# Kernel tuning notes

Hardware: AMD Instinct MI355X
Metric: run time of the kernel (lower is better)

## Reference

```python
import jax, jax.numpy as jnp
import numpy as np

B, Dx, Dz, Dy, H = 4096, 512, 512, 256, 2048
T0, T1 = 0.0, 1.0
N_STEPS = 64


def setup_inputs() -> dict:
    key = jax.random.key(0)
    ks = jax.random.split(key, 9)
    X = jax.random.normal(ks[0], (B, Dx), jnp.float32)
    # P sampled Uniform(0.01, 0.1) as in the torch module
    P = jax.random.uniform(ks[1], (Dz, Dx), jnp.float32, 0.01, 0.1)
    # A scaled so spectral radius ~1 -> exp(A*T) stays bounded over the integration
    A = jax.random.normal(ks[2], (Dz, Dz), jnp.float32) * (Dz ** -0.5)
    W1 = jax.random.normal(ks[3], (H, Dz), jnp.float32) * (Dz ** -0.5)
    b1 = jax.random.normal(ks[4], (H,), jnp.float32) * 0.01
    W2 = jax.random.normal(ks[5], (H, H), jnp.float32) * (H ** -0.5)
    b2 = jax.random.normal(ks[6], (H,), jnp.float32) * 0.01
    W3 = jax.random.normal(ks[7], (Dy, H), jnp.float32) * (H ** -0.5)
    b3 = jax.random.normal(ks[8], (Dy,), jnp.float32) * 0.01
    return dict(X=X, P=P, A=A, W1=W1, b1=b1, W2=W2, b2=b2, W3=W3, b3=b3,
                n_steps=N_STEPS)


def reference(X, P, A, W1, b1, W2, b2, W3, b3, n_steps):
    # Z0 = einsum('ji,bi->bj', P, X)  -> projection into latent ODE state
    z0 = X @ P.T  # [B, Dz]
    dt = jnp.float32((T1 - T0) / n_steps)

    def f(z):  # dz/dt = A z, batched: einsum('ji,bi->bj', A, z)
        return z @ A.T

    def rk4_step(z, _):
        k1 = f(z)
        k2 = f(z + 0.5 * dt * k1)
        k3 = f(z + 0.5 * dt * k2)
        k4 = f(z + dt * k3)
        return z + (dt / 6.0) * (k1 + 2.0 * k2 + 2.0 * k3 + k4), None

    zT, _ = jax.lax.scan(rk4_step, z0, None, length=n_steps)  # [B, Dz]

    # QnnMatrixODE MLP head (n_layers=3): Lin+ReLU, Lin+ReLU, Lin
    h = jax.nn.relu(zT @ W1.T + b1)
    h = jax.nn.relu(h @ W2.T + b2)
    y = h @ W3.T + b3  # [B, Dy]
    return y
```

## Files before the change

### kernel.cpp

```cpp
#include <hip/hip_runtime.h>

#define BDIM 4096
#define DX 512
#define DZ 512
#define DY 256
#define HD 2048
#define LDT 72

typedef __attribute__((ext_vector_type(8))) short bf16x8;
typedef __attribute__((ext_vector_type(4))) float f32x4;

__device__ inline unsigned short f2bf(float f) {
    unsigned u = __float_as_uint(f);
    unsigned r = 0x7FFFu + ((u >> 16) & 1u);
    return (unsigned short)((u + r) >> 16);
}
__device__ inline float bf2f(unsigned short h) {
    return __uint_as_float(((unsigned)h) << 16);
}

#define GLDS16(g, l)                                                            \
    __builtin_amdgcn_global_load_lds((const __attribute__((address_space(1))) void*)(g), \
                                     (__attribute__((address_space(3))) void*)(l), 16, 0, 0)

struct PrepJobs {
    const float* src[7];
    unsigned short* hi[7];
    unsigned short* lo[7];
    int n4[7];
};
__global__ __launch_bounds__(256) void prep_k(PrepJobs J) {
    const int j = blockIdx.y;
    if (j < 6) {
        const int i4 = blockIdx.x * 256 + threadIdx.x;
        if (i4 >= J.n4[j]) return;
        float4 v = ((const float4*)J.src[j])[i4];
        ushort4 h;
        h.x = f2bf(v.x); h.y = f2bf(v.y); h.z = f2bf(v.z); h.w = f2bf(v.w);
        ((ushort4*)J.hi[j])[i4] = h;
        if (J.lo[j]) {
            ushort4 l;
            l.x = f2bf(v.x - bf2f(h.x));
            l.y = f2bf(v.y - bf2f(h.y));
            l.z = f2bf(v.z - bf2f(h.z));
            l.w = f2bf(v.w - bf2f(h.w));
            ((ushort4*)J.lo[j])[i4] = l;
        }
    } else {
        if (blockIdx.x >= 256) return;
        __shared__ float t[32][33];
        const float* A = J.src[6];
        unsigned short* HT = J.hi[6];
        unsigned short* LT = J.lo[6];
        const int bx = (blockIdx.x & 15) * 32, by = (blockIdx.x >> 4) * 32;
        const int x = threadIdx.x & 31, y = threadIdx.x >> 5;
#pragma unroll
        for (int dy = 0; dy < 32; dy += 8)
            t[y + dy][x] = A[(size_t)(by + y + dy) * DZ + bx + x];
        __syncthreads();
#pragma unroll
        for (int dy = 0; dy < 32; dy += 8) {
            float v = t[x][y + dy];
            unsigned short h = f2bf(v);
            size_t o = (size_t)(bx + y + dy) * DZ + by + x;
            HT[o] = h;
            LT[o] = f2bf(v - bf2f(h));
        }
    }
}

struct G64In { const unsigned short *Ahi, *Alo, *Bhi, *Blo; const float* Dadd; };
struct G64Out { float* Cf32; unsigned short *Chi, *Clo, *CThi, *CTlo; };
struct E0Out {
    const float* Af32;
    const unsigned short *A2h, *A2l;
    unsigned short *B0Th, *B0Tl, *B1Th, *B1Tl, *B2Th, *B2Tl;
};

template <int EPI>
__device__ __forceinline__ void g64_core(int bx, int by, int M, int N, int K,
                                         G64In in, G64Out o, E0Out e,
                                         unsigned short* Ash, unsigned short* Asl,
                                         unsigned short* Bsh, unsigned short* Bsl) {
    const int tid = threadIdx.x;
    const int lane = tid & 63;
    const int wave = tid >> 6;
    const int wr = wave >> 1, wc = wave & 1;
    const int row0 = by * 64, col0 = bx * 64;
    const int sr = tid >> 2;
    const int sk = (tid & 3) * 16;

    const int niter = K >> 6;
    bf16x8 pa0, pa1, pl0, pl1, pb0, pb1, pq0, pq1;
    {
        const unsigned short* ar = in.Ahi + (size_t)(row0 + sr) * K + sk;
        const unsigned short* al = in.Alo + (size_t)(row0 + sr) * K + sk;
        const unsigned short* br = in.Bhi + (size_t)(col0 + sr) * K + sk;
        const unsigned short* bl = in.Blo + (size_t)(col0 + sr) * K + sk;
        pa0 = *(const bf16x8*)ar; pa1 = *(const bf16x8*)(ar + 8);
        pl0 = *(const bf16x8*)al; pl1 = *(const bf16x8*)(al + 8);
        pb0 = *(const bf16x8*)br; pb1 = *(const bf16x8*)(br + 8);
        pq0 = *(const bf16x8*)bl; pq1 = *(const bf16x8*)(bl + 8);
    }

    f32x4 acc[4] = {};
    const int mb = wr * 32 + (lane & 15);
    const int nb = wc * 32 + (lane & 15);

    for (int it = 0; it < niter; ++it) {
        __syncthreads();
        *(bf16x8*)&Ash[sr * LDT + sk] = pa0; *(bf16x8*)&Ash[sr * LDT + sk + 8] = pa1;
        *(bf16x8*)&Asl[sr * LDT + sk] = pl0; *(bf16x8*)&Asl[sr * LDT + sk + 8] = pl1;
        *(bf16x8*)&Bsh[sr * LDT + sk] = pb0; *(bf16x8*)&Bsh[sr * LDT + sk + 8] = pb1;
        *(bf16x8*)&Bsl[sr * LDT + sk] = pq0; *(bf16x8*)&Bsl[sr * LDT + sk + 8] = pq1;
        __syncthreads();

        {
            const int kn = (it + 1 < niter) ? ((it + 1) << 6) : 0;
            const unsigned short* ar = in.Ahi + (size_t)(row0 + sr) * K + kn + sk;
            const unsigned short* al = in.Alo + (size_t)(row0 + sr) * K + kn + sk;
            const unsigned short* br = in.Bhi + (size_t)(col0 + sr) * K + kn + sk;
            const unsigned short* bl = in.Blo + (size_t)(col0 + sr) * K + kn + sk;
            pa0 = *(const bf16x8*)ar; pa1 = *(const bf16x8*)(ar + 8);
            pl0 = *(const bf16x8*)al; pl1 = *(const bf16x8*)(al + 8);
            pb0 = *(const bf16x8*)br; pb1 = *(const bf16x8*)(br + 8);
            pq0 = *(const bf16x8*)bl; pq1 = *(const bf16x8*)(bl + 8);
        }

#pragma unroll
        for (int kh = 0; kh < 2; ++kh) {
            const int kk = kh * 32 + (lane >> 4) * 8;
            bf16x8 ah[2], alx[2], bh[2], blx[2];
#pragma unroll
            for (int t = 0; t < 2; ++t) {
                ah[t]  = *(const bf16x8*)&Ash[(mb + t * 16) * LDT + kk];
                alx[t] = *(const bf16x8*)&Asl[(mb + t * 16) * LDT + kk];
                bh[t]  = *(const bf16x8*)&Bsh[(nb + t * 16) * LDT + kk];
                blx[t] = *(const bf16x8*)&Bsl[(nb + t * 16) * LDT + kk];
            }
#pragma unroll
            for (int mt = 0; mt < 2; ++mt)
#pragma unroll
                for (int nt = 0; nt < 2; ++nt) {
                    acc[mt * 2 + nt] = __builtin_amdgcn_mfma_f32_16x16x32_bf16(
                        ah[mt], bh[nt], acc[mt * 2 + nt], 0, 0, 0);
                    acc[mt * 2 + nt] = __builtin_amdgcn_mfma_f32_16x16x32_bf16(
                        ah[mt], blx[nt], acc[mt * 2 + nt], 0, 0, 0);
                    acc[mt * 2 + nt] = __builtin_amdgcn_mfma_f32_16x16x32_bf16(
                        alx[mt], bh[nt], acc[mt * 2 + nt], 0, 0, 0);
                }
        }
    }

#pragma unroll
    for (int mt = 0; mt < 2; ++mt) {
        const int grow = row0 + wr * 32 + mt * 16 + (lane >> 4) * 4;
#pragma unroll
        for (int nt = 0; nt < 2; ++nt) {
            const int gcol = col0 + wc * 32 + nt * 16 + (lane & 15);
            f32x4 a = acc[mt * 2 + nt];
            if (EPI == 1) {
                ushort4 h0, l0, h1v, l1v, h2v, l2v;
                unsigned short* H0 = &h0.x;  unsigned short* L0 = &l0.x;
                unsigned short* H1 = &h1v.x; unsigned short* L1 = &l1v.x;
                unsigned short* H2 = &h2v.x; unsigned short* L2 = &l2v.x;
#pragma unroll
                for (int i = 0; i < 4; ++i) {
                    const size_t idx = (size_t)(grow + i) * N + gcol;
                    const float di = (grow + i == gcol) ? 1.0f : 0.0f;
                    const float av = e.Af32[idx];
                    const float a2v = bf2f(e.A2h[idx]) + bf2f(e.A2l[idx]);
                    const float a3v = a[i];
                    float b0 = di + av + 0.5f * a2v + 1.6666667e-1f * a3v;
                    float b1 = 4.1666668e-2f * di + 8.3333333e-3f * av +
                               1.3888889e-3f * a2v + 1.9841270e-4f * a3v;
                    float b2 = 2.4801587e-5f * di + 2.7557319e-6f * av +
                               2.7557319e-7f * a2v + 2.5052108e-8f * a3v;
                    H0[i] = f2bf(b0); L0[i] = f2bf(b0 - bf2f(H0[i]));
                    H1[i] = f2bf(b1); L1[i] = f2bf(b1 - bf2f(H1[i]));
                    H2[i] = f2bf(b2); L2[i] = f2bf(b2 - bf2f(H2[i]));
                }
                const size_t to = (size_t)gcol * DZ + grow;
                *(ushort4*)&e.B0Th[to] = h0; *(ushort4*)&e.B0Tl[to] = l0;
                *(ushort4*)&e.B1Th[to] = h1v; *(ushort4*)&e.B1Tl[to] = l1v;
                *(ushort4*)&e.B2Th[to] = h2v; *(ushort4*)&e.B2Tl[to] = l2v;
            } else {
                if (in.Dadd) {
#pragma unroll
                    for (int i = 0; i < 4; ++i)
                        a[i] += in.Dadd[(size_t)(grow + i) * N + gcol];
                }
                unsigned short h4[4], l4[4];
#pragma unroll
                for (int i = 0; i < 4; ++i) {
                    h4[i] = f2bf(a[i]);
                    l4[i] = f2bf(a[i] - bf2f(h4[i]));
                }
                if (o.Cf32) {
#pragma unroll
                    for (int i = 0; i < 4; ++i) o.Cf32[(size_t)(grow + i) * N + gcol] = a[i];
                }
                if (o.Chi) {
#pragma unroll
                    for (int i = 0; i < 4; ++i) o.Chi[(size_t)(grow + i) * N + gcol] = h4[i];
                }
                if (o.Clo) {
#pragma unroll
                    for (int i = 0; i < 4; ++i) o.Clo[(size_t)(grow + i) * N + gcol] = l4[i];
                }
                if (o.CThi) {
                    ushort4 u = {h4[0], h4[1], h4[2], h4[3]};
                    *(ushort4*)&o.CThi[(size_t)gcol * M + grow] = u;
                }
                if (o.CTlo) {
                    ushort4 u = {l4[0], l4[1], l4[2], l4[3]};
                    *(ushort4*)&o.CTlo[(size_t)gcol * M + grow] = u;
                }
            }
        }
    }
}

__global__ __launch_bounds__(256) void g64_one(G64In in, G64Out o, int M, int N, int K) {
    __shared__ __align__(16) unsigned short Ash[64 * LDT], Asl[64 * LDT];
    __shared__ __align__(16) unsigned short Bsh[64 * LDT], Bsl[64 * LDT];
    E0Out e = {};
    g64_core<0>(blockIdx.x, blockIdx.y, M, N, K, in, o, e, Ash, Asl, Bsh, Bsl);
}

__global__ __launch_bounds__(256) void g64_dual_e0(G64In i0, E0Out e0o,
                                                   G64In i1, G64Out o1) {
    __shared__ __align__(16) unsigned short Ash[64 * LDT], Asl[64 * LDT];
    __shared__ __align__(16) unsigned short Bsh[64 * LDT], Bsl[64 * LDT];
    if (blockIdx.z == 0) {
        G64Out on = {};
        g64_core<1>(blockIdx.x, blockIdx.y, DZ, DZ, DZ, i0, on, e0o, Ash, Asl, Bsh, Bsl);
    } else {
        E0Out en = {};
        g64_core<0>(blockIdx.x, blockIdx.y, DZ, DZ, DZ, i1, o1, en, Ash, Asl, Bsh, Bsl);
    }
}

__global__ __launch_bounds__(256) void g64_tri(G64In i0, G64Out o0, G64In i1, G64Out o1,
                                               G64In i2, G64Out o2, int M, int N, int K) {
    __shared__ __align__(16) unsigned short Ash[64 * LDT], Asl[64 * LDT];
    __shared__ __align__(16) unsigned short Bsh[64 * LDT], Bsl[64 * LDT];
    E0Out e = {};
    G64In in = (blockIdx.z == 0) ? i0 : (blockIdx.z == 1) ? i1 : i2;
    G64Out o = (blockIdx.z == 0) ? o0 : (blockIdx.z == 1) ? o1 : o2;
    g64_core<0>(blockIdx.x, blockIdx.y, M, N, K, in, o, e, Ash, Asl, Bsh, Bsl);
}

template <int RELU, int BIAS, int OUT_BF16>
__global__ __launch_bounds__(256) void gemm_bf16_v2(int M, int N, int K,
                                                    const unsigned short* __restrict__ A,
                                                    const unsigned short* __restrict__ B,
                                                    void* __restrict__ C,
                                                    const float* __restrict__ bias) {
    __shared__ unsigned short As[64 * 32];
    __shared__ unsigned short Bs[128 * 32];

    const int tid = threadIdx.x;
    const int lane = tid & 63;
    const int wave = tid >> 6;
    const int wr = wave >> 1, wc = wave & 1;
    const int row0 = blockIdx.y * 64;
    const int col0 = blockIdx.x * 128;

    const int srow = lane >> 2;
    const int schunk = (lane & 3) * 8;

    f32x4 acc[2][4] = {};

    for (int k0 = 0; k0 < K; k0 += 32) {
        GLDS16(A + (size_t)(row0 + wave * 16 + srow) * K + k0 + schunk, &As[(wave * 16) * 32]);
        GLDS16(B + (size_t)(col0 + wave * 32 + srow) * K + k0 + schunk, &Bs[(wave * 32) * 32]);
        GLDS16(B + (size_t)(col0 + wave * 32 + 16 + srow) * K + k0 + schunk,
               &Bs[(wave * 32 + 16) * 32]);
        __syncthreads();

        const int kk = (lane >> 4) * 8;
        const int mbase = wr * 32 + (lane & 15);
        const int nbase = wc * 64 + (lane & 15);
        bf16x8 af[2], bf[4];
#pragma unroll
        for (int t = 0; t < 2; ++t) af[t] = *(const bf16x8*)&As[(mbase + t * 16) * 32 + kk];
#pragma unroll
        for (int t = 0; t < 4; ++t) bf[t] = *(const bf16x8*)&Bs[(nbase + t * 16) * 32 + kk];
#pragma unroll
        for (int mt = 0; mt < 2; ++mt)
#pragma unroll
            for (int nt = 0; nt < 4; ++nt)
                acc[mt][nt] = __builtin_amdgcn_mfma_f32_16x16x32_bf16(af[mt], bf[nt],
                                                                      acc[mt][nt], 0, 0, 0);
        __syncthreads();
    }

#pragma unroll
    for (int mt = 0; mt < 2; ++mt) {
        const int grow = row0 + wr * 32 + mt * 16 + (lane >> 4) * 4;
#pragma unroll
        for (int nt = 0; nt < 4; ++nt) {
            const int gcol = col0 + wc * 64 + nt * 16 + (lane & 15);
            const float bv = BIAS ? bias[gcol] : 0.0f;
#pragma unroll
            for (int i = 0; i < 4; ++i) {
                float v = acc[mt][nt][i] + bv;
                if (RELU) v = fmaxf(v, 0.0f);
                const size_t off = (size_t)(grow + i) * N + gcol;
                if (OUT_BF16)
                    ((unsigned short*)C)[off] = f2bf(v);
                else
                    ((float*)C)[off] = v;
            }
        }
    }
}

__global__ __launch_bounds__(256) void gemm64nt_y(int M, int N, int K,
                                                  const unsigned short* __restrict__ A,
                                                  const unsigned short* __restrict__ B,
                                                  float* __restrict__ C,
                                                  const float* __restrict__ bias) {
    __shared__ __align__(16) unsigned short As[64 * LDT];
    __shared__ __align__(16) unsigned short Bs[64 * LDT];
    const int tid = threadIdx.x;
    const int lane = tid & 63;
    const int wave = tid >> 6;
    const int wr = wave >> 1, wc = wave & 1;
    const int row0 = blockIdx.y * 64;
    const int col0 = blockIdx.x * 64;
    const int sr = tid >> 2, sk = (tid & 3) * 16;

    const int niter = K >> 6;
    bf16x8 pa0, pa1, pb0, pb1;
    {
        const unsigned short* ar = A + (size_t)(row0 + sr) * K + sk;
        const unsigned short* br = B + (size_t)(col0 + sr) * K + sk;
        pa0 = *(const bf16x8*)ar; pa1 = *(const bf16x8*)(ar + 8);
        pb0 = *(const bf16x8*)br; pb1 = *(const bf16x8*)(br + 8);
    }

    f32x4 acc[4] = {};
    const int mb = wr * 32 + (lane & 15);
    const int nb = wc * 32 + (lane & 15);

    for (int it = 0; it < niter; ++it) {
        __syncthreads();
        *(bf16x8*)&As[sr * LDT + sk] = pa0; *(bf16x8*)&As[sr * LDT + sk + 8] = pa1;
        *(bf16x8*)&Bs[sr * LDT + sk] = pb0; *(bf16x8*)&Bs[sr * LDT + sk + 8] = pb1;
        __syncthreads();

        {
            const int kn = (it + 1 < niter) ? ((it + 1) << 6) : 0;
            const unsigned short* ar = A + (size_t)(row0 + sr) * K + kn + sk;
            const unsigned short* br = B + (size_t)(col0 + sr) * K + kn + sk;
            pa0 = *(const bf16x8*)ar; pa1 = *(const bf16x8*)(ar + 8);
            pb0 = *(const bf16x8*)br; pb1 = *(const bf16x8*)(br + 8);
        }

#pragma unroll
        for (int kh = 0; kh < 2; ++kh) {
            const int kk = kh * 32 + (lane >> 4) * 8;
            bf16x8 af[2], bf[2];
#pragma unroll
            for (int t = 0; t < 2; ++t) {
                af[t] = *(const bf16x8*)&As[(mb + t * 16) * LDT + kk];
                bf[t] = *(const bf16x8*)&Bs[(nb + t * 16) * LDT + kk];
            }
#pragma unroll
            for (int mt = 0; mt < 2; ++mt)
#pragma unroll
                for (int nt = 0; nt < 2; ++nt)
                    acc[mt * 2 + nt] = __builtin_amdgcn_mfma_f32_16x16x32_bf16(
                        af[mt], bf[nt], acc[mt * 2 + nt], 0, 0, 0);
        }
    }

#pragma unroll
    for (int mt = 0; mt < 2; ++mt) {
        const int grow = row0 + wr * 32 + mt * 16 + (lane >> 4) * 4;
#pragma unroll
        for (int nt = 0; nt < 2; ++nt) {
            const int gcol = col0 + wc * 32 + nt * 16 + (lane & 15);
            const float bv = bias ? bias[gcol] : 0.0f;
#pragma unroll
            for (int i = 0; i < 4; ++i)
                C[(size_t)(grow + i) * N + gcol] = acc[mt * 2 + nt][i] + bv;
        }
    }
}

extern "C" void kernel_launch(void* const* d_in, const int* in_sizes, int n_in,
                              void* d_out, int out_size, void* d_ws, size_t ws_size,
                              hipStream_t stream) {
    const float* X  = (const float*)d_in[0];
    const float* P  = (const float*)d_in[1];
    const float* Am = (const float*)d_in[2];
    const float* W1 = (const float*)d_in[3];
    const float* b1 = (const float*)d_in[4];
    const float* W2 = (const float*)d_in[5];
    const float* b2 = (const float*)d_in[6];
    const float* W3 = (const float*)d_in[7];
    const float* b3 = (const float*)d_in[8];
    float* out = (float*)d_out;

    const size_t S = (size_t)DZ * DZ;
    const size_t SW = (size_t)HD * DZ;

    char* p = (char*)d_ws;
    auto alloc_f = [&](size_t n) { float* r = (float*)p; p += n * 4; return r; };
    auto alloc_h = [&](size_t n) { unsigned short* r = (unsigned short*)p; p += ((n * 2 + 15) & ~15ull); return r; };
    unsigned short* Xb   = alloc_h((size_t)BDIM * DX);
    unsigned short* W2b  = alloc_h((size_t)HD * HD);
    unsigned short* W3b  = alloc_h((size_t)DY * HD);
    unsigned short* W1h  = alloc_h(SW);
    unsigned short* W1l  = alloc_h(SW);
    unsigned short* Pb   = alloc_h(S);
    unsigned short* Ah   = alloc_h(S);
    unsigned short* Al   = alloc_h(S);
    unsigned short* ATh  = alloc_h(S);
    unsigned short* ATl  = alloc_h(S);
    unsigned short* A2h  = alloc_h(S);
    unsigned short* A2l  = alloc_h(S);
    unsigned short* A2Th = alloc_h(S);
    unsigned short* A2Tl = alloc_h(S);
    unsigned short* A4Th = alloc_h(S);
    unsigned short* A4Tl = alloc_h(S);
    unsigned short* B0Th = alloc_h(S);
    unsigned short* B0Tl = alloc_h(S);
    unsigned short* B1Th = alloc_h(S);
    unsigned short* B1Tl = alloc_h(S);
    unsigned short* B2Th = alloc_h(S);
    unsigned short* B2Tl = alloc_h(S);
    float* U0f = alloc_f(SW);
    float* U1f = alloc_f(SW);
    unsigned short* U2h  = alloc_h(SW);
    unsigned short* U2l  = alloc_h(SW);
    unsigned short* Vh   = alloc_h(SW);
    unsigned short* Vl   = alloc_h(SW);
    unsigned short* C1b  = alloc_h(SW);
    unsigned short* XPb  = alloc_h((size_t)BDIM * DZ);
    unsigned short* h1b  = alloc_h((size_t)BDIM * HD);
    unsigned short* h2b  = alloc_h((size_t)BDIM * HD);

    PrepJobs J;
    J.src[0] = X;  J.hi[0] = Xb;  J.lo[0] = nullptr; J.n4[0] = BDIM * DX / 4;
    J.src[1] = W2; J.hi[1] = W2b; J.lo[1] = nullptr; J.n4[1] = HD * HD / 4;
    J.src[2] = W3; J.hi[2] = W3b; J.lo[2] = nullptr; J.n4[2] = DY * HD / 4;
    J.src[3] = W1; J.hi[3] = W1h; J.lo[3] = W1l;     J.n4[3] = (int)(SW / 4);
    J.src[4] = Am; J.hi[4] = Ah;  J.lo[4] = Al;      J.n4[4] = (int)(S / 4);
    J.src[5] = P;  J.hi[5] = Pb;  J.lo[5] = nullptr; J.n4[5] = (int)(S / 4);
    J.src[6] = Am; J.hi[6] = ATh; J.lo[6] = ATl;     J.n4[6] = 256;
    prep_k<<<dim3(HD * HD / 4 / 256, 7), 256, 0, stream>>>(J);

    gemm_bf16_v2<0, 0, 1><<<dim3(DZ / 128, BDIM / 64), 256, 0, stream>>>(
        BDIM, DZ, DX, Xb, Pb, XPb, nullptr);

    dim3 g8(DZ / 64, DZ / 64);

    {
        G64In i{Ah, Al, ATh, ATl, nullptr};
        G64Out o{nullptr, A2h, A2l, A2Th, A2Tl};
        g64_one<<<g8, 256, 0, stream>>>(i, o, DZ, DZ, DZ);
    }
    {
        G64In i0{A2h, A2l, ATh, ATl, nullptr};
        E0Out e0o{Am, A2h, A2l, B0Th, B0Tl, B1Th, B1Tl, B2Th, B2Tl};
        G64In i1{A2h, A2l, A2Th, A2Tl, nullptr};
        G64Out o1{nullptr, nullptr, nullptr, A4Th, A4Tl};
        g64_dual_e0<<<dim3(DZ / 64, DZ / 64, 2), 256, 0, stream>>>(i0, e0o, i1, o1);
    }
    {
        G64In i0{W1h, W1l, B0Th, B0Tl, nullptr};
        G64Out o0{U0f, nullptr, nullptr, nullptr, nullptr};
        G64In i1{W1h, W1l, B1Th, B1Tl, nullptr};
        G64Out o1{U1f, nullptr, nullptr, nullptr, nullptr};
        G64In i2{W1h, W1l, B2Th, B2Tl, nullptr};
        G64Out o2{nullptr, U2h, U2l, nullptr, nullptr};
        g64_tri<<<dim3(DZ / 64, HD / 64, 3), 256, 0, stream>>>(i0, o0, i1, o1, i2, o2,
                                                               HD, DZ, DZ);
    }
    {
        G64In i{U2h, U2l, A4Th, A4Tl, U1f};
        G64Out o{nullptr, Vh, Vl, nullptr, nullptr};
        g64_one<<<dim3(DZ / 64, HD / 64), 256, 0, stream>>>(i, o, HD, DZ, DZ);
    }
    {
        G64In i{Vh, Vl, A4Th, A4Tl, U0f};
        G64Out o{nullptr, C1b, nullptr, nullptr, nullptr};
        g64_one<<<dim3(DZ / 64, HD / 64), 256, 0, stream>>>(i, o, HD, DZ, DZ);
    }

    gemm_bf16_v2<1, 1, 1><<<dim3(HD / 128, BDIM / 64), 256, 0, stream>>>(
        BDIM, HD, DZ, XPb, C1b, h1b, b1);
    gemm_bf16_v2<1, 1, 1><<<dim3(HD / 128, BDIM / 64), 256, 0, stream>>>(
        BDIM, HD, HD, h1b, W2b, h2b, b2);
    gemm64nt_y<<<dim3(DY / 64, BDIM / 64), 256, 0, stream>>>(
        BDIM, DY, HD, h2b, W3b, out, b3);
}
```

Measured before the change: 263.6 us.

## Merge setup GEMMs into combined launches and replace serial Horner chain with A^8 path

The X·P projection and the A² computation now share one launch. A⁸ is computed alongside the three W1·B products in a four-way batched launch. The two dependent Horner-style GEMMs (U2·A4 + U1, then V·A4 + U0) become one kernel that accumulates U1·A4 and U2·A8 into the same accumulator and adds U0. The goal is fewer launches and a shorter serial dependency chain, at the cost of extra A⁴/A⁸ products and U1 stored as a hi/lo split. U0 is aliased into the Ah buffer, which is dead by then, to save workspace.

```diff
diff --git a/kernel.cpp b/kernel.cpp
--- a/kernel.cpp
+++ b/kernel.cpp
@@ -77,6 +77,69 @@
     unsigned short *B0Th, *B0Tl, *B1Th, *B1Tl, *B2Th, *B2Tl;
 };
 
+__device__ __forceinline__ void g64_kloop(G64In in, int row0, int col0, int K,
+                                          f32x4 (&acc)[4], int sr, int sk, int mb, int nb,
+                                          unsigned short* Ash, unsigned short* Asl,
+                                          unsigned short* Bsh, unsigned short* Bsl) {
+    const int niter = K >> 6;
+    bf16x8 pa0, pa1, pl0, pl1, pb0, pb1, pq0, pq1;
+    {
+        const unsigned short* ar = in.Ahi + (size_t)(row0 + sr) * K + sk;
+        const unsigned short* al = in.Alo + (size_t)(row0 + sr) * K + sk;
+        const unsigned short* br = in.Bhi + (size_t)(col0 + sr) * K + sk;
+        const unsigned short* bl = in.Blo + (size_t)(col0 + sr) * K + sk;
+        pa0 = *(const bf16x8*)ar; pa1 = *(const bf16x8*)(ar + 8);
+        pl0 = *(const bf16x8*)al; pl1 = *(const bf16x8*)(al + 8);
+        pb0 = *(const bf16x8*)br; pb1 = *(const bf16x8*)(br + 8);
+        pq0 = *(const bf16x8*)bl; pq1 = *(const bf16x8*)(bl + 8);
+    }
+
+    for (int it = 0; it < niter; ++it) {
+        __syncthreads();
+        *(bf16x8*)&Ash[sr * LDT + sk] = pa0; *(bf16x8*)&Ash[sr * LDT + sk + 8] = pa1;
+        *(bf16x8*)&Asl[sr * LDT + sk] = pl0; *(bf16x8*)&Asl[sr * LDT + sk + 8] = pl1;
+        *(bf16x8*)&Bsh[sr * LDT + sk] = pb0; *(bf16x8*)&Bsh[sr * LDT + sk + 8] = pb1;
+        *(bf16x8*)&Bsl[sr * LDT + sk] = pq0; *(bf16x8*)&Bsl[sr * LDT + sk + 8] = pq1;
+        __syncthreads();
+
+        {
+            const int kn = (it + 1 < niter) ? ((it + 1) << 6) : 0;
+            const unsigned short* ar = in.Ahi + (size_t)(row0 + sr) * K + kn + sk;
+            const unsigned short* al = in.Alo + (size_t)(row0 + sr) * K + kn + sk;
+            const unsigned short* br = in.Bhi + (size_t)(col0 + sr) * K + kn + sk;
+            const unsigned short* bl = in.Blo + (size_t)(col0 + sr) * K + kn + sk;
+            pa0 = *(const bf16x8*)ar; pa1 = *(const bf16x8*)(ar + 8);
+            pl0 = *(const bf16x8*)al; pl1 = *(const bf16x8*)(al + 8);
+            pb0 = *(const bf16x8*)br; pb1 = *(const bf16x8*)(br + 8);
+            pq0 = *(const bf16x8*)bl; pq1 = *(const bf16x8*)(bl + 8);
+        }
+
+#pragma unroll
+        for (int kh = 0; kh < 2; ++kh) {
+            const int kk = kh * 32 + (threadIdx.x >> 4 & 3) * 8;
+            bf16x8 ah[2], alx[2], bh[2], blx[2];
+#pragma unroll
+            for (int t = 0; t < 2; ++t) {
+                ah[t]  = *(const bf16x8*)&Ash[(mb + t * 16) * LDT + kk];
+                alx[t] = *(const bf16x8*)&Asl[(mb + t * 16) * LDT + kk];
+                bh[t]  = *(const bf16x8*)&Bsh[(nb + t * 16) * LDT + kk];
+                blx[t] = *(const bf16x8*)&Bsl[(nb + t * 16) * LDT + kk];
+            }
+#pragma unroll
+            for (int mt = 0; mt < 2; ++mt)
+#pragma unroll
+                for (int nt = 0; nt < 2; ++nt) {
+                    acc[mt * 2 + nt] = __builtin_amdgcn_mfma_f32_16x16x32_bf16(
+                        ah[mt], bh[nt], acc[mt * 2 + nt], 0, 0, 0);
+                    acc[mt * 2 + nt] = __builtin_amdgcn_mfma_f32_16x16x32_bf16(
+                        ah[mt], blx[nt], acc[mt * 2 + nt], 0, 0, 0);
+                    acc[mt * 2 + nt] = __builtin_amdgcn_mfma_f32_16x16x32_bf16(
+                        alx[mt], bh[nt], acc[mt * 2 + nt], 0, 0, 0);
+                }
+        }
+    }
+}
+
 template <int EPI>
 __device__ __forceinline__ void g64_core(int bx, int by, int M, int N, int K,
                                          G64In in, G64Out o, E0Out e,
@@ -89,68 +152,11 @@
     const int row0 = by * 64, col0 = bx * 64;
     const int sr = tid >> 2;
     const int sk = (tid & 3) * 16;
-
-    const int niter = K >> 6;
-    bf16x8 pa0, pa1, pl0, pl1, pb0, pb1, pq0, pq1;
-    {
-        const unsigned short* ar = in.Ahi + (size_t)(row0 + sr) * K + sk;
-        const unsigned short* al = in.Alo + (size_t)(row0 + sr) * K + sk;
-        const unsigned short* br = in.Bhi + (size_t)(col0 + sr) * K + sk;
-        const unsigned short* bl = in.Blo + (size_t)(col0 + sr) * K + sk;
-        pa0 = *(const bf16x8*)ar; pa1 = *(const bf16x8*)(ar + 8);
-        pl0 = *(const bf16x8*)al; pl1 = *(const bf16x8*)(al + 8);
-        pb0 = *(const bf16x8*)br; pb1 = *(const bf16x8*)(br + 8);
-        pq0 = *(const bf16x8*)bl; pq1 = *(const bf16x8*)(bl + 8);
-    }
-
-    f32x4 acc[4] = {};
     const int mb = wr * 32 + (lane & 15);
     const int nb = wc * 32 + (lane & 15);
 
-    for (int it = 0; it < niter; ++it) {
-        __syncthreads();
-        *(bf16x8*)&Ash[sr * LDT + sk] = pa0; *(bf16x8*)&Ash[sr * LDT + sk + 8] = pa1;
-        *(bf16x8*)&Asl[sr * LDT + sk] = pl0; *(bf16x8*)&Asl[sr * LDT + sk + 8] = pl1;
-        *(bf16x8*)&Bsh[sr * LDT + sk] = pb0; *(bf16x8*)&Bsh[sr * LDT + sk + 8] = pb1;
-        *(bf16x8*)&Bsl[sr * LDT + sk] = pq0; *(bf16x8*)&Bsl[sr * LDT + sk + 8] = pq1;
-        __syncthreads();
-
-        {
-            const int kn = (it + 1 < niter) ? ((it + 1) << 6) : 0;
-            const unsigned short* ar = in.Ahi + (size_t)(row0 + sr) * K + kn + sk;
-            const unsigned short* al = in.Alo + (size_t)(row0 + sr) * K + kn + sk;
-            const unsigned short* br = in.Bhi + (size_t)(col0 + sr) * K + kn + sk;
-            const unsigned short* bl = in.Blo + (size_t)(col0 + sr) * K + kn + sk;
-            pa0 = *(const bf16x8*)ar; pa1 = *(const bf16x8*)(ar + 8);
-            pl0 = *(const bf16x8*)al; pl1 = *(const bf16x8*)(al + 8);
-            pb0 = *(const bf16x8*)br; pb1 = *(const bf16x8*)(br + 8);
-            pq0 = *(const bf16x8*)bl; pq1 = *(const bf16x8*)(bl + 8);
-        }
-
-#pragma unroll
-        for (int kh = 0; kh < 2; ++kh) {
-            const int kk = kh * 32 + (lane >> 4) * 8;
-            bf16x8 ah[2], alx[2], bh[2], blx[2];
-#pragma unroll
-            for (int t = 0; t < 2; ++t) {
-                ah[t]  = *(const bf16x8*)&Ash[(mb + t * 16) * LDT + kk];
-                alx[t] = *(const bf16x8*)&Asl[(mb + t * 16) * LDT + kk];
-                bh[t]  = *(const bf16x8*)&Bsh[(nb + t * 16) * LDT + kk];
-                blx[t] = *(const bf16x8*)&Bsl[(nb + t * 16) * LDT + kk];
-            }
-#pragma unroll
-            for (int mt = 0; mt < 2; ++mt)
-#pragma unroll
-                for (int nt = 0; nt < 2; ++nt) {
-                    acc[mt * 2 + nt] = __builtin_amdgcn_mfma_f32_16x16x32_bf16(
-                        ah[mt], bh[nt], acc[mt * 2 + nt], 0, 0, 0);
-                    acc[mt * 2 + nt] = __builtin_amdgcn_mfma_f32_16x16x32_bf16(
-                        ah[mt], blx[nt], acc[mt * 2 + nt], 0, 0, 0);
-                    acc[mt * 2 + nt] = __builtin_amdgcn_mfma_f32_16x16x32_bf16(
-                        alx[mt], bh[nt], acc[mt * 2 + nt], 0, 0, 0);
-                }
-        }
-    }
+    f32x4 acc[4] = {};
+    g64_kloop(in, row0, col0, K, acc, sr, sk, mb, nb, Ash, Asl, Bsh, Bsl);
 
 #pragma unroll
     for (int mt = 0; mt < 2; ++mt) {
@@ -221,11 +227,96 @@
     }
 }
 
-__global__ __launch_bounds__(256) void g64_one(G64In in, G64Out o, int M, int N, int K) {
-    __shared__ __align__(16) unsigned short Ash[64 * LDT], Asl[64 * LDT];
-    __shared__ __align__(16) unsigned short Bsh[64 * LDT], Bsl[64 * LDT];
-    E0Out e = {};
-    g64_core<0>(blockIdx.x, blockIdx.y, M, N, K, in, o, e, Ash, Asl, Bsh, Bsl);
+template <int RELU, int BIAS, int OUT_BF16>
+__device__ __forceinline__ void bigemm_core(int bxi, int byi, int M, int N, int K,
+                                            const unsigned short* __restrict__ A,
+                                            const unsigned short* __restrict__ B,
+                                            void* __restrict__ C,
+                                            const float* __restrict__ bias,
+                                            unsigned short* As, unsigned short* Bs) {
+    const int tid = threadIdx.x;
+    const int lane = tid & 63;
+    const int wave = tid >> 6;
+    const int wr = wave >> 1, wc = wave & 1;
+    const int row0 = byi * 64;
+    const int col0 = bxi * 128;
+
+    const int srow = lane >> 2;
+    const int schunk = (lane & 3) * 8;
+
+    f32x4 acc[2][4] = {};
+
+    for (int k0 = 0; k0 < K; k0 += 32) {
+        GLDS16(A + (size_t)(row0 + wave * 16 + srow) * K + k0 + schunk, &As[(wave * 16) * 32]);
+        GLDS16(B + (size_t)(col0 + wave * 32 + srow) * K + k0 + schunk, &Bs[(wave * 32) * 32]);
+        GLDS16(B + (size_t)(col0 + wave * 32 + 16 + srow) * K + k0 + schunk,
+               &Bs[(wave * 32 + 16) * 32]);
+        __syncthreads();
+
+        const int kk = (lane >> 4) * 8;
+        const int mbase = wr * 32 + (lane & 15);
+        const int nbase = wc * 64 + (lane & 15);
+        bf16x8 af[2], bf[4];
+#pragma unroll
+        for (int t = 0; t < 2; ++t) af[t] = *(const bf16x8*)&As[(mbase + t * 16) * 32 + kk];
+#pragma unroll
+        for (int t = 0; t < 4; ++t) bf[t] = *(const bf16x8*)&Bs[(nbase + t * 16) * 32 + kk];
+#pragma unroll
+        for (int mt = 0; mt < 2; ++mt)
+#pragma unroll
+            for (int nt = 0; nt < 4; ++nt)
+                acc[mt][nt] = __builtin_amdgcn_mfma_f32_16x16x32_bf16(af[mt], bf[nt],
+                                                                      acc[mt][nt], 0, 0, 0);
+        __syncthreads();
+    }
+
+#pragma unroll
+    for (int mt = 0; mt < 2; ++mt) {
+        const int grow = row0 + wr * 32 + mt * 16 + (lane >> 4) * 4;
+#pragma unroll
+        for (int nt = 0; nt < 4; ++nt) {
+            const int gcol = col0 + wc * 64 + nt * 16 + (lane & 15);
+            const float bv = BIAS ? bias[gcol] : 0.0f;
+#pragma unroll
+            for (int i = 0; i < 4; ++i) {
+                float v = acc[mt][nt][i] + bv;
+                if (RELU) v = fmaxf(v, 0.0f);
+                const size_t off = (size_t)(grow + i) * N + gcol;
+                if (OUT_BF16)
+                    ((unsigned short*)C)[off] = f2bf(v);
+                else
+                    ((float*)C)[off] = v;
+            }
+        }
+    }
+}
+
+template <int RELU, int BIAS, int OUT_BF16>
+__global__ __launch_bounds__(256) void gemm_bf16_v2(int M, int N, int K,
+                                                    const unsigned short* __restrict__ A,
+                                                    const unsigned short* __restrict__ B,
+                                                    void* __restrict__ C,
+                                                    const float* __restrict__ bias) {
+    __shared__ unsigned short As[64 * 32];
+    __shared__ unsigned short Bs[128 * 32];
+    bigemm_core<RELU, BIAS, OUT_BF16>(blockIdx.x, blockIdx.y, M, N, K, A, B, C, bias, As, Bs);
+}
+
+__global__ __launch_bounds__(256) void combo_k(const unsigned short* Xb,
+                                               const unsigned short* Pb,
+                                               unsigned short* XPb,
+                                               G64In ia, G64Out oa) {
+    __shared__ __align__(16) unsigned short smem[4 * 64 * LDT];
+    if (blockIdx.z == 0) {
+        if (blockIdx.x >= DZ / 128) return;
+        bigemm_core<0, 0, 1>(blockIdx.x, blockIdx.y, BDIM, DZ, DX, Xb, Pb, XPb, nullptr,
+                             smem, smem + 64 * 32);
+    } else {
+        if (blockIdx.x >= 8 || blockIdx.y >= 8) return;
+        E0Out e = {};
+        g64_core<0>(blockIdx.x, blockIdx.y, DZ, DZ, DZ, ia, oa, e,
+                    smem, smem + 64 * LDT, smem + 128 * LDT, smem + 192 * LDT);
+    }
 }
 
 __global__ __launch_bounds__(256) void g64_dual_e0(G64In i0, E0Out e0o,
@@ -241,77 +332,47 @@
     }
 }
 
-__global__ __launch_bounds__(256) void g64_tri(G64In i0, G64Out o0, G64In i1, G64Out o1,
-                                               G64In i2, G64Out o2, int M, int N, int K) {
+__global__ __launch_bounds__(256) void g64_quad(G64In i0, G64Out o0, G64In i1, G64Out o1,
+                                                G64In i2, G64Out o2, G64In i3, G64Out o3) {
     __shared__ __align__(16) unsigned short Ash[64 * LDT], Asl[64 * LDT];
     __shared__ __align__(16) unsigned short Bsh[64 * LDT], Bsl[64 * LDT];
+    const int z = blockIdx.z;
+    if (z == 3 && blockIdx.y >= 8) return;
+    G64In in = (z == 0) ? i0 : (z == 1) ? i1 : (z == 2) ? i2 : i3;
+    G64Out o = (z == 0) ? o0 : (z == 1) ? o1 : (z == 2) ? o2 : o3;
+    const int M = (z < 3) ? HD : DZ;
     E0Out e = {};
-    G64In in = (blockIdx.z == 0) ? i0 : (blockIdx.z == 1) ? i1 : i2;
-    G64Out o = (blockIdx.z == 0) ? o0 : (blockIdx.z == 1) ? o1 : o2;
-    g64_core<0>(blockIdx.x, blockIdx.y, M, N, K, in, o, e, Ash, Asl, Bsh, Bsl);
-}
-
-template <int RELU, int BIAS, int OUT_BF16>
-__global__ __launch_bounds__(256) void gemm_bf16_v2(int M, int N, int K,
-                                                    const unsigned short* __restrict__ A,
-                                                    const unsigned short* __restrict__ B,
-                                                    void* __restrict__ C,
-                                                    const float* __restrict__ bias) {
-    __shared__ unsigned short As[64 * 32];
-    __shared__ unsigned short Bs[128 * 32];
-
+    g64_core<0>(blockIdx.x, blockIdx.y, M, DZ, DZ, in, o, e, Ash, Asl, Bsh, Bsl);
+}
+
+__global__ __launch_bounds__(256) void g64_c1(G64In s1, G64In s2,
+                                              const float* __restrict__ U0,
+                                              unsigned short* __restrict__ C1b) {
+    __shared__ __align__(16) unsigned short Ash[64 * LDT], Asl[64 * LDT];
+    __shared__ __align__(16) unsigned short Bsh[64 * LDT], Bsl[64 * LDT];
     const int tid = threadIdx.x;
     const int lane = tid & 63;
     const int wave = tid >> 6;
     const int wr = wave >> 1, wc = wave & 1;
-    const int row0 = blockIdx.y * 64;
-    const int col0 = blockIdx.x * 128;
-
-    const int srow = lane >> 2;
-    const int schunk = (lane & 3) * 8;
-
-    f32x4 acc[2][4] = {};
-
-    for (int k0 = 0; k0 < K; k0 += 32) {
-        GLDS16(A + (size_t)(row0 + wave * 16 + srow) * K + k0 + schunk, &As[(wave * 16) * 32]);
-        GLDS16(B + (size_t)(col0 + wave * 32 + srow) * K + k0 + schunk, &Bs[(wave * 32) * 32]);
-        GLDS16(B + (size_t)(col0 + wave * 32 + 16 + srow) * K + k0 + schunk,
-               &Bs[(wave * 32 + 16) * 32]);
-        __syncthreads();
-
-        const int kk = (lane >> 4) * 8;
-        const int mbase = wr * 32 + (lane & 15);
-        const int nbase = wc * 64 + (lane & 15);
-        bf16x8 af[2], bf[4];
-#pragma unroll
-        for (int t = 0; t < 2; ++t) af[t] = *(const bf16x8*)&As[(mbase + t * 16) * 32 + kk];
-#pragma unroll
-        for (int t = 0; t < 4; ++t) bf[t] = *(const bf16x8*)&Bs[(nbase + t * 16) * 32 + kk];
-#pragma unroll
-        for (int mt = 0; mt < 2; ++mt)
-#pragma unroll
-            for (int nt = 0; nt < 4; ++nt)
-                acc[mt][nt] = __builtin_amdgcn_mfma_f32_16x16x32_bf16(af[mt], bf[nt],
-                                                                      acc[mt][nt], 0, 0, 0);
-        __syncthreads();
-    }
+    const int row0 = blockIdx.y * 64, col0 = blockIdx.x * 64;
+    const int sr = tid >> 2, sk = (tid & 3) * 16;
+    const int mb = wr * 32 + (lane & 15);
+    const int nb = wc * 32 + (lane & 15);
+
+    f32x4 acc[4] = {};
+    g64_kloop(s1, row0, col0, DZ, acc, sr, sk, mb, nb, Ash, Asl, Bsh, Bsl);
+    g64_kloop(s2, row0, col0, DZ, acc, sr, sk, mb, nb, Ash, Asl, Bsh, Bsl);
 
 #pragma unroll
     for (int mt = 0; mt < 2; ++mt) {
         const int grow = row0 + wr * 32 + mt * 16 + (lane >> 4) * 4;
 #pragma unroll
-        for (int nt = 0; nt < 4; ++nt) {
-            const int gcol = col0 + wc * 64 + nt * 16 + (lane & 15);
-            const float bv = BIAS ? bias[gcol] : 0.0f;
+        for (int nt = 0; nt < 2; ++nt) {
+            const int gcol = col0 + wc * 32 + nt * 16 + (lane & 15);
 #pragma unroll
             for (int i = 0; i < 4; ++i) {
-                float v = acc[mt][nt][i] + bv;
-                if (RELU) v = fmaxf(v, 0.0f);
-                const size_t off = (size_t)(grow + i) * N + gcol;
-                if (OUT_BF16)
-                    ((unsigned short*)C)[off] = f2bf(v);
-                else
-                    ((float*)C)[off] = v;
+                const size_t idx = (size_t)(grow + i) * DZ + gcol;
+                C1b[idx] = f2bf(acc[mt * 2 + nt][i] + U0[idx]);
             }
         }
     }
@@ -409,7 +470,6 @@
     const size_t SW = (size_t)HD * DZ;
 
     char* p = (char*)d_ws;
-    auto alloc_f = [&](size_t n) { float* r = (float*)p; p += n * 4; return r; };
     auto alloc_h = [&](size_t n) { unsigned short* r = (unsigned short*)p; p += ((n * 2 + 15) & ~15ull); return r; };
     unsigned short* Xb   = alloc_h((size_t)BDIM * DX);
     unsigned short* W2b  = alloc_h((size_t)HD * HD);
@@ -425,24 +485,27 @@
     unsigned short* A2l  = alloc_h(S);
     unsigned short* A2Th = alloc_h(S);
     unsigned short* A2Tl = alloc_h(S);
+    unsigned short* A4h  = alloc_h(S);
+    unsigned short* A4l  = alloc_h(S);
     unsigned short* A4Th = alloc_h(S);
     unsigned short* A4Tl = alloc_h(S);
+    unsigned short* A8Th = alloc_h(S);
+    unsigned short* A8Tl = alloc_h(S);
     unsigned short* B0Th = alloc_h(S);
     unsigned short* B0Tl = alloc_h(S);
     unsigned short* B1Th = alloc_h(S);
     unsigned short* B1Tl = alloc_h(S);
     unsigned short* B2Th = alloc_h(S);
     unsigned short* B2Tl = alloc_h(S);
-    float* U0f = alloc_f(SW);
-    float* U1f = alloc_f(SW);
+    unsigned short* U1h  = alloc_h(SW);
+    unsigned short* U1l  = alloc_h(SW);
     unsigned short* U2h  = alloc_h(SW);
     unsigned short* U2l  = alloc_h(SW);
-    unsigned short* Vh   = alloc_h(SW);
-    unsigned short* Vl   = alloc_h(SW);
     unsigned short* C1b  = alloc_h(SW);
     unsigned short* XPb  = alloc_h((size_t)BDIM * DZ);
     unsigned short* h1b  = alloc_h((size_t)BDIM * HD);
     unsigned short* h2b  = alloc_h((size_t)BDIM * HD);
+    float* U0f = (float*)Ah;
 
     PrepJobs J;
     J.src[0] = X;  J.hi[0] = Xb;  J.lo[0] = nullptr; J.n4[0] = BDIM * DX / 4;
@@ -454,42 +517,33 @@
     J.src[6] = Am; J.hi[6] = ATh; J.lo[6] = ATl;     J.n4[6] = 256;
     prep_k<<<dim3(HD * HD / 4 / 256, 7), 256, 0, stream>>>(J);
 
-    gemm_bf16_v2<0, 0, 1><<<dim3(DZ / 128, BDIM / 64), 256, 0, stream>>>(
-        BDIM, DZ, DX, Xb, Pb, XPb, nullptr);
-
-    dim3 g8(DZ / 64, DZ / 64);
-
     {
-        G64In i{Ah, Al, ATh, ATl, nullptr};
-        G64Out o{nullptr, A2h, A2l, A2Th, A2Tl};
-        g64_one<<<g8, 256, 0, stream>>>(i, o, DZ, DZ, DZ);
+        G64In ia{Ah, Al, ATh, ATl, nullptr};
+        G64Out oa{nullptr, A2h, A2l, A2Th, A2Tl};
+        combo_k<<<dim3(8, BDIM / 64, 2), 256, 0, stream>>>(Xb, Pb, XPb, ia, oa);
     }
     {
         G64In i0{A2h, A2l, ATh, ATl, nullptr};
         E0Out e0o{Am, A2h, A2l, B0Th, B0Tl, B1Th, B1Tl, B2Th, B2Tl};
         G64In i1{A2h, A2l, A2Th, A2Tl, nullptr};
-        G64Out o1{nullptr, nullptr, nullptr, A4Th, A4Tl};
+        G64Out o1{nullptr, A4h, A4l, A4Th, A4Tl};
         g64_dual_e0<<<dim3(DZ / 64, DZ / 64, 2), 256, 0, stream>>>(i0, e0o, i1, o1);
     }
     {
         G64In i0{W1h, W1l, B0Th, B0Tl, nullptr};
         G64Out o0{U0f, nullptr, nullptr, nullptr, nullptr};
         G64In i1{W1h, W1l, B1Th, B1Tl, nullptr};
-        G64Out o1{U1f, nullptr, nullptr, nullptr, nullptr};
+        G64Out o1{nullptr, U1h, U1l, nullptr, nullptr};
         G64In i2{W1h, W1l, B2Th, B2Tl, nullptr};
         G64Out o2{nullptr, U2h, U2l, nullptr, nullptr};
-        g64_tri<<<dim3(DZ / 64, HD / 64, 3), 256, 0, stream>>>(i0, o0, i1, o1, i2, o2,
-                                                               HD, DZ, DZ);
+        G64In i3{A4h, A4l, A4Th, A4Tl, nullptr};
+        G64Out o3{nullptr, nullptr, nullptr, A8Th, A8Tl};
+        g64_quad<<<dim3(DZ / 64, HD / 64, 4), 256, 0, stream>>>(i0, o0, i1, o1, i2, o2, i3, o3);
     }
     {
-        G64In i{U2h, U2l, A4Th, A4Tl, U1f};
-        G64Out o{nullptr, Vh, Vl, nullptr, nullptr};
-        g64_one<<<dim3(DZ / 64, HD / 64), 256, 0, stream>>>(i, o, HD, DZ, DZ);
-    }
-    {
-        G64In i{Vh, Vl, A4Th, A4Tl, U0f};
-        G64Out o{nullptr, C1b, nullptr, nullptr, nullptr};
-        g64_one<<<dim3(DZ / 64, HD / 64), 256, 0, stream>>>(i, o, HD, DZ, DZ);
+        G64In s1{U1h, U1l, A4Th, A4Tl, nullptr};
+        G64In s2{U2h, U2l, A8Th, A8Tl, nullptr};
+        g64_c1<<<dim3(DZ / 64, HD / 64), 256, 0, stream>>>(s1, s2, U0f, C1b);
     }
 
     gemm_bf16_v2<1, 1, 1><<<dim3(HD / 128, BDIM / 64), 256, 0, stream>>>(
```

New measurement: 258.6 us. No clear change (-1.9%).
